# Kernel tuning notes

Hardware: AMD Instinct MI355X
Metric: run time of the kernel (lower is better)

## Reference

```python
import jax, jax.numpy as jnp
import numpy as np

N, E, IN, H, C = 50000, 1600000, 256, 256, 2


def _lin(k, o, i):
    return (jax.random.normal(k, (o, i), jnp.float32) / np.sqrt(i)).astype(jnp.float32)


def setup_inputs() -> dict:
    key = jax.random.key(0)
    ks = jax.random.split(key, 16)
    x = jax.random.normal(ks[0], (N, IN), jnp.float32)
    edge_index = jax.random.randint(ks[1], (2, E), 0, N, dtype=jnp.int32)
    return dict(
        x=x, edge_index=edge_index,
        W1=_lin(ks[2], H, IN), b1=0.01 * jax.random.normal(ks[10], (H,), jnp.float32),
        W2=_lin(ks[3], H, H), b2=0.01 * jax.random.normal(ks[11], (H,), jnp.float32),
        W3=_lin(ks[4], H, H), b3=0.01 * jax.random.normal(ks[12], (H,), jnp.float32),
        W4=_lin(ks[5], C, H), b4=0.01 * jax.random.normal(ks[13], (C,), jnp.float32),
        T10=_lin(ks[6], H, H), T11=_lin(ks[7], H, H), cb1=0.01 * jax.random.normal(ks[14], (H,), jnp.float32),
        T20=_lin(ks[8], H, H), T21=_lin(ks[9], H, H), cb2=0.01 * jax.random.normal(ks[15], (H,), jnp.float32),
    )


def _cheb_norm(edge_index, n):
    # PyG ChebConv, normalization='sym', lambda_max=2.0:
    # L_hat = 2/lambda_max * (I - D^-1/2 A D^-1/2) - I = -D^-1/2 A D^-1/2
    # (the +I and -I self-loop terms cancel), so only off-diagonal norm remains.
    row, col = edge_index[0], edge_index[1]
    deg = jax.ops.segment_sum(jnp.ones((edge_index.shape[1],), jnp.float32), row, num_segments=n)
    dis = jnp.where(deg > 0, jax.lax.rsqrt(jnp.where(deg > 0, deg, 1.0)), 0.0)
    return -dis[row] * dis[col]  # [E]


def _cheb_conv(x, edge_index, norm, W0, W1, b, n):
    # K=2: out = Tx_0 @ W0^T + Tx_1 @ W1^T + b, Tx_0 = x, Tx_1 = L_hat x
    src, dst = edge_index[0], edge_index[1]  # message: x_j from src, aggregate at dst
    tx1 = jax.ops.segment_sum(norm[:, None] * x[src], dst, num_segments=n)
    return x @ W0.T + tx1 @ W1.T + b


def reference(x, edge_index, W1, b1, W2, b2, W3, b3, W4, b4, T10, T11, cb1, T20, T21, cb2):
    n = x.shape[0]
    norm = _cheb_norm(edge_index, n)
    h = jax.nn.relu(x @ W1.T + b1)
    h = jax.nn.relu(h @ W2.T + b2)
    h = _cheb_conv(h, edge_index, norm, T10, T11, cb1, n)
    h = _cheb_conv(h, edge_index, norm, T20, T21, cb2, n)
    h = jax.nn.relu(h @ W3.T + b3)
    return h @ W4.T + b4
```

## Files before the change

kernel.cpp:

```cpp
#include <hip/hip_runtime.h>

#define HDIM 256
#define NHB 256
#define NBINB 50048
#define NBINW (NBINB/4)
#define NBAND 16
#define LDP 40

typedef __attribute__((ext_vector_type(8))) short short8v;
typedef __attribute__((ext_vector_type(4))) short short4v;
typedef __attribute__((ext_vector_type(4))) float floatx4;

static __device__ __forceinline__ unsigned short f2bf(float f) {
    union { float f; unsigned u; } c; c.f = f;
    unsigned u = c.u;
    unsigned r = u + 0x7FFFu + ((u >> 16) & 1u);
    return (unsigned short)(r >> 16);
}
static __device__ __forceinline__ float bf2f(unsigned short h) {
    union { unsigned u; float f; } c; c.u = ((unsigned)h) << 16;
    return c.f;
}


__global__ __launch_bounds__(512) void hist_k(const int* __restrict__ src, const int* __restrict__ dst,
                                              unsigned int* __restrict__ degS, unsigned int* __restrict__ cntS,
                                              int nE) {
    __shared__ unsigned int h8[NBINW];
    const int tid = threadIdx.x;
    const int isDst = blockIdx.x >= NHB;
    const int bb = isDst ? blockIdx.x - NHB : blockIdx.x;
    const int* __restrict__ arr = isDst ? dst : src;
    unsigned int* __restrict__ outS = isDst ? cntS : degS;

    for (int i = tid; i < NBINW; i += 512) h8[i] = 0u;
    __syncthreads();
    const int chunk = (nE + NHB - 1) / NHB;
    const int e0 = bb * chunk;
    const int e1 = min(e0 + chunk, nE);
    for (int e = e0 + tid; e < e1; e += 512) {
        int n = arr[e];
        atomicAdd(&h8[n >> 2], 1u << ((n & 3) << 3));
    }
    __syncthreads();
    unsigned int* __restrict__ row = outS + (size_t)bb * NBINW;
    for (int i = tid; i < NBINW; i += 512) row[i] = h8[i];
}


__global__ __launch_bounds__(256) void reduce_k(const unsigned char* __restrict__ degS,
                                                unsigned char* __restrict__ cntS,
                                                float* __restrict__ dis, int* __restrict__ tmp,
                                                int* __restrict__ bsums, int nN) {
    __shared__ int s[256];
    const int t = threadIdx.x;
    const int n = blockIdx.x * 256 + t;
    int run = 0;
    if (n < nN) {
        int d = 0;
        #pragma unroll 8
        for (int b = 0; b < NHB; ++b) d += degS[(size_t)b * NBINB + n];
        dis[n] = (d > 0) ? (1.0f / sqrtf((float)d)) : 0.0f;
        unsigned r = 0;
        #pragma unroll 4
        for (int b = 0; b < NHB; ++b) {
            size_t o = (size_t)b * NBINB + n;
            unsigned c = cntS[o];
            cntS[o] = (unsigned char)r;
            r += c;
        }
        run = (int)r;
    }
    s[t] = run; __syncthreads();
    #pragma unroll
    for (int off = 1; off < 256; off <<= 1) {
        int x = (t >= off) ? s[t - off] : 0;
        __syncthreads();
        s[t] += x;
        __syncthreads();
    }
    if (n < nN) tmp[n] = s[t];
    if (t == 255) bsums[blockIdx.x] = s[255];
}


__global__ __launch_bounds__(256) void scan3_k(const int* __restrict__ tmp, const int* __restrict__ bsums,
                                               int* __restrict__ offs, int nN, int nE, int nb) {
    __shared__ int s[256];
    const int t = threadIdx.x;
    int v = (t < nb) ? bsums[t] : 0;
    s[t] = v; __syncthreads();
    #pragma unroll
    for (int off = 1; off < 256; off <<= 1) {
        int x = (t >= off) ? s[t - off] : 0;
        __syncthreads();
        s[t] += x;
        __syncthreads();
    }
    const int base = (blockIdx.x > 0) ? s[blockIdx.x - 1] : 0;
    __syncthreads();
    const int i = blockIdx.x * 256 + t;
    if (i < nN) {
        int prev = (t > 0) ? tmp[i - 1] : 0;
        offs[i] = base + prev;
    }
    if (i == nN - 1) offs[nN] = nE;
}


__global__ __launch_bounds__(512) void fill_k(const int* __restrict__ src, const int* __restrict__ dst,
                                              const float* __restrict__ dis, const int* __restrict__ offs,
                                              const unsigned int* __restrict__ cntS,
                                              int2* __restrict__ csr, int nE) {
    __shared__ unsigned int cur8[NBINW];
    const int tid = threadIdx.x;
    const int bb = blockIdx.x;
    const unsigned int* __restrict__ baseRow = cntS + (size_t)bb * NBINW;
    for (int i = tid; i < NBINW; i += 512) cur8[i] = baseRow[i];
    __syncthreads();
    const int chunk = (nE + NHB - 1) / NHB;
    const int e0 = bb * chunk;
    const int e1 = min(e0 + chunk, nE);
    for (int e = e0 + tid; e < e1; e += 512) {
        int s = src[e], d = dst[e];
        unsigned sh = (unsigned)(d & 3) << 3;
        unsigned old = atomicAdd(&cur8[d >> 2], 1u << sh);
        unsigned c = (old >> sh) & 0xFFu;
        int p = offs[d] + (int)c;
        float w = -dis[s] * dis[d];
        csr[p] = make_int2(s, __float_as_int(w));
    }
}


struct WPtrs { const float* w[7]; };
__global__ __launch_bounds__(256) void wsplit_all_k(WPtrs ws, unsigned short* __restrict__ base) {
    int wi = blockIdx.x >> 6;
    int idx = (blockIdx.x & 63) * 256 + threadIdx.x;
    const float* w = ws.w[wi];
    unsigned short* hi = base + (size_t)wi * 131072;
    unsigned short* lo = hi + 65536;
    float4 v = ((const float4*)w)[idx];
    float f[4] = {v.x, v.y, v.z, v.w};
    short4v hv, lv;
    #pragma unroll
    for (int e = 0; e < 4; ++e) {
        unsigned short h = f2bf(f[e]);
        float rem = f[e] - bf2f(h);
        hv[e] = (short)h;
        lv[e] = (short)f2bf(rem);
    }
    *(short4v*)(hi + idx * 4) = hv;
    *(short4v*)(lo + idx * 4) = lv;
}


__global__ __launch_bounds__(512, 4) void mfma_gemm_k(
    const float* __restrict__ AF,
    const unsigned short* __restrict__ Ah0, const unsigned short* __restrict__ Al0,
    const unsigned short* __restrict__ Wh0, const unsigned short* __restrict__ Wl0,
    const unsigned short* __restrict__ Ah1, const unsigned short* __restrict__ Al1,
    const unsigned short* __restrict__ Wh1, const unsigned short* __restrict__ Wl1,
    const float* __restrict__ bias,
    float* __restrict__ outF, unsigned short* __restrict__ outHi, unsigned short* __restrict__ outLo,
    signed char* __restrict__ outI8, float* __restrict__ outSc,
    const float* __restrict__ W4f, const float* __restrict__ b4f, float* __restrict__ outFinal,
    int nRows, int relu, int dual)
{
    __shared__ short Ahs[128 * LDP];
    __shared__ short Als[128 * LDP];
    __shared__ short Bhs[256 * LDP];
    __shared__ short Bls[256 * LDP];

    const int tid  = threadIdx.x;
    const int lane = tid & 63;
    const int wv   = tid >> 6;
    const int wm   = wv >> 2, wn = wv & 3;
    const int lrow = lane & 15, kg = lane >> 4;
    const int row0 = blockIdx.x * 128;

    const int sr = tid >> 2, sc = tid & 3;
    int agr = row0 + sr; if (agr >= nRows) agr = nRows - 1;

    floatx4 acc[4][4];
    #pragma unroll
    for (int i = 0; i < 4; ++i)
        #pragma unroll
        for (int j = 0; j < 4; ++j)
            acc[i][j] = (floatx4)0.0f;

    const int npass = dual ? 2 : 1;
    for (int pass = 0; pass < npass; ++pass) {
        const unsigned short* __restrict__ Ah = pass ? Ah1 : Ah0;
        const unsigned short* __restrict__ Al = pass ? Al1 : Al0;
        const unsigned short* __restrict__ Wh = pass ? Wh1 : Wh0;
        const unsigned short* __restrict__ Wl = pass ? Wl1 : Wl0;
        const bool f32A = (pass == 0) && (AF != nullptr);
        for (int k0 = 0; k0 < HDIM; k0 += 32) {
            __syncthreads();
            if (f32A) {
                const float* pa = AF + (size_t)agr * HDIM + k0 + sc * 8;
                float4 v0 = *(const float4*)pa;
                float4 v1 = *(const float4*)(pa + 4);
                float f[8] = {v0.x, v0.y, v0.z, v0.w, v1.x, v1.y, v1.z, v1.w};
                short8v hv, lv;
                #pragma unroll
                for (int e = 0; e < 8; ++e) {
                    unsigned short h = f2bf(f[e]);
                    float rem = f[e] - bf2f(h);
                    hv[e] = (short)h;
                    lv[e] = (short)f2bf(rem);
                }
                *(short8v*)(Ahs + sr * LDP + sc * 8) = hv;
                *(short8v*)(Als + sr * LDP + sc * 8) = lv;
            } else {
                size_t ga = (size_t)agr * HDIM + k0 + sc * 8;
                *(short8v*)(Ahs + sr * LDP + sc * 8) = *(const short8v*)(Ah + ga);
                *(short8v*)(Als + sr * LDP + sc * 8) = *(const short8v*)(Al + ga);
            }
            #pragma unroll
            for (int q = 0; q < 2; ++q) {
                int idx = tid + q * 512;
                int br = idx >> 2, bc = idx & 3;
                size_t gb = (size_t)br * HDIM + k0 + bc * 8;
                *(short8v*)(Bhs + br * LDP + bc * 8) = *(const short8v*)(Wh + gb);
                *(short8v*)(Bls + br * LDP + bc * 8) = *(const short8v*)(Wl + gb);
            }
            __syncthreads();

            short8v ahf[4], alf[4];
            #pragma unroll
            for (int fm = 0; fm < 4; ++fm) {
                int ra = (wm * 64 + fm * 16 + lrow) * LDP + kg * 8;
                ahf[fm] = *(const short8v*)(Ahs + ra);
                alf[fm] = *(const short8v*)(Als + ra);
            }
            #pragma unroll
            for (int fn = 0; fn < 4; ++fn) {
                int rb = (wn * 64 + fn * 16 + lrow) * LDP + kg * 8;
                short8v bh = *(const short8v*)(Bhs + rb);
                short8v bl = *(const short8v*)(Bls + rb);
                #pragma unroll
                for (int fm = 0; fm < 4; ++fm) {
                    acc[fm][fn] = __builtin_amdgcn_mfma_f32_16x16x32_bf16(ahf[fm], bh, acc[fm][fn], 0, 0, 0);
                    acc[fm][fn] = __builtin_amdgcn_mfma_f32_16x16x32_bf16(ahf[fm], bl, acc[fm][fn], 0, 0, 0);
                    acc[fm][fn] = __builtin_amdgcn_mfma_f32_16x16x32_bf16(alf[fm], bh, acc[fm][fn], 0, 0, 0);
                }
            }
        }
    }

    if (outFinal) {
        float w40[4], w41[4];
        #pragma unroll
        for (int fn = 0; fn < 4; ++fn) {
            int col = wn * 64 + fn * 16 + lrow;
            w40[fn] = W4f[col];
            w41[fn] = W4f[HDIM + col];
        }
        float p0[4][4], p1[4][4];
        #pragma unroll
        for (int fm = 0; fm < 4; ++fm)
            #pragma unroll
            for (int r = 0; r < 4; ++r) { p0[fm][r] = 0.f; p1[fm][r] = 0.f; }
        #pragma unroll
        for (int fn = 0; fn < 4; ++fn) {
            int col = wn * 64 + fn * 16 + lrow;
            float bv = bias[col];
            #pragma unroll
            for (int fm = 0; fm < 4; ++fm)
                #pragma unroll
                for (int r = 0; r < 4; ++r) {
                    float v = fmaxf(acc[fm][fn][r] + bv, 0.0f);
                    p0[fm][r] = fmaf(v, w40[fn], p0[fm][r]);
                    p1[fm][r] = fmaf(v, w41[fn], p1[fm][r]);
                }
        }
        #pragma unroll
        for (int fm = 0; fm < 4; ++fm)
            #pragma unroll
            for (int r = 0; r < 4; ++r) {
                #pragma unroll
                for (int m = 1; m < 16; m <<= 1) {
                    p0[fm][r] += __shfl_xor(p0[fm][r], m, 64);
                    p1[fm][r] += __shfl_xor(p1[fm][r], m, 64);
                }
            }
        __syncthreads();
        float* red = (float*)Ahs;
        if (lrow == 0) {
            #pragma unroll
            for (int fm = 0; fm < 4; ++fm)
                #pragma unroll
                for (int r = 0; r < 4; ++r) {
                    int rl = wm * 64 + fm * 16 + kg * 4 + r;
                    red[(wn * 128 + rl) * 2 + 0] = p0[fm][r];
                    red[(wn * 128 + rl) * 2 + 1] = p1[fm][r];
                }
        }
        __syncthreads();
        if (tid < 256) {
            int rl = tid >> 1, j = tid & 1;
            int grow = row0 + rl;
            if (grow < nRows) {
                float s = b4f[j]
                        + red[(0 * 128 + rl) * 2 + j] + red[(1 * 128 + rl) * 2 + j]
                        + red[(2 * 128 + rl) * 2 + j] + red[(3 * 128 + rl) * 2 + j];
                outFinal[(size_t)grow * 2 + j] = s;
            }
        }
        return;
    }

    float vmax[4][4];
    #pragma unroll
    for (int fm = 0; fm < 4; ++fm)
        #pragma unroll
        for (int r = 0; r < 4; ++r) vmax[fm][r] = 0.0f;
    #pragma unroll
    for (int fn = 0; fn < 4; ++fn) {
        int col = wn * 64 + fn * 16 + lrow;
        float bv = bias[col];
        #pragma unroll
        for (int fm = 0; fm < 4; ++fm) {
            #pragma unroll
            for (int r = 0; r < 4; ++r) {
                float v = acc[fm][fn][r] + bv;
                if (relu) v = fmaxf(v, 0.0f);
                vmax[fm][r] = fmaxf(vmax[fm][r], fabsf(v));
                int grow = row0 + wm * 64 + fm * 16 + kg * 4 + r;
                if (grow < nRows) {
                    size_t o = (size_t)grow * HDIM + col;
                    if (outF) outF[o] = v;
                    if (outHi) {
                        unsigned short h = f2bf(v);
                        outHi[o] = h;
                        outLo[o] = f2bf(v - bf2f(h));
                    }
                }
            }
        }
    }

    if (outI8) {
        #pragma unroll
        for (int fm = 0; fm < 4; ++fm)
            #pragma unroll
            for (int r = 0; r < 4; ++r) {
                #pragma unroll
                for (int m = 1; m < 16; m <<= 1)
                    vmax[fm][r] = fmaxf(vmax[fm][r], __shfl_xor(vmax[fm][r], m, 64));
            }
        __syncthreads();
        float* wmax = (float*)Ahs;
        if (lrow == 0) {
            #pragma unroll
            for (int fm = 0; fm < 4; ++fm)
                #pragma unroll
                for (int r = 0; r < 4; ++r) {
                    int rl = wm * 64 + fm * 16 + kg * 4 + r;
                    wmax[wn * 128 + rl] = vmax[fm][r];
                }
        }
        __syncthreads();
        #pragma unroll
        for (int fm = 0; fm < 4; ++fm) {
            #pragma unroll
            for (int r = 0; r < 4; ++r) {
                int rl = wm * 64 + fm * 16 + kg * 4 + r;
                int grow = row0 + rl;
                float rmax = fmaxf(fmaxf(wmax[rl], wmax[128 + rl]),
                                   fmaxf(wmax[256 + rl], wmax[384 + rl]));
                float inv = (rmax > 0.0f) ? (127.0f / rmax) : 0.0f;
                if (grow < nRows) {
                    #pragma unroll
                    for (int fn = 0; fn < 4; ++fn) {
                        int col = wn * 64 + fn * 16 + lrow;
                        float v = acc[fm][fn][r] + bias[col];
                        if (relu) v = fmaxf(v, 0.0f);
                        outI8[(size_t)grow * HDIM + col] = (signed char)(int)rintf(v * inv);
                    }
                    if (wn == 0 && lrow == 0) outSc[grow] = rmax * (1.0f / 127.0f);
                }
            }
        }
    }
}


#define ACCQ1(m)                                                                 \
    {                                                                            \
        unsigned pv = *(const unsigned*)(hq + (size_t)m.x * HDIM + lane * 4);    \
        float wq = __int_as_float(m.y) * hs[m.x];                                \
        a0 = fmaf(wq, (float)((int)(pv << 24) >> 24), a0);                       \
        a1 = fmaf(wq, (float)((int)(pv << 16) >> 24), a1);                       \
        a2 = fmaf(wq, (float)((int)(pv << 8) >> 24), a2);                        \
        a3 = fmaf(wq, (float)((int)pv >> 24), a3);                               \
    }

#define ACCQ4(m0, m1, m2, m3) { ACCQ1(m0); ACCQ1(m1); ACCQ1(m2); ACCQ1(m3); }

__global__ __launch_bounds__(256) void aggregate_k(
    const signed char* __restrict__ hq, const float* __restrict__ hs,
    const int2* __restrict__ csr, const int* __restrict__ offs,
    unsigned short* __restrict__ outHi, unsigned short* __restrict__ outLo)
{
    __shared__ float red[4][256];
    __shared__ int2 sorted[256];
    __shared__ unsigned bins[NBAND];
    __shared__ unsigned cur[NBAND];

    const int n = blockIdx.x;
    const int tid = threadIdx.x;
    const int w = tid >> 6;
    const int lane = tid & 63;
    const int start = offs[n], end = offs[n + 1];
    const int deg = end - start;

    float a0 = 0.f, a1 = 0.f, a2 = 0.f, a3 = 0.f;

    if (deg <= 256) {
        if (tid < NBAND) { bins[tid] = 0u; }
        __syncthreads();
        int2 my; int myband = 0;
        if (tid < deg) {
            my = csr[start + tid];
            myband = my.x >> 12;
            atomicAdd(&bins[myband], 1u);
        }
        __syncthreads();
        if (tid == 0) {
            unsigned run = 0;
            #pragma unroll
            for (int b = 0; b < NBAND; ++b) { unsigned c = bins[b]; cur[b] = run; run += c; }
        }
        __syncthreads();
        if (tid < deg) {
            unsigned pos = atomicAdd(&cur[myband], 1u);
            sorted[pos] = my;
        }
        __syncthreads();

        int e = w;
        for (; e + 12 < deg; e += 16) {
            int2 m0 = sorted[e], m1 = sorted[e + 4], m2 = sorted[e + 8], m3 = sorted[e + 12];
            ACCQ4(m0, m1, m2, m3);
        }
        for (; e < deg; e += 4) {
            int2 m = sorted[e];
            ACCQ1(m);
        }
    } else {
        int e = start + w;
        for (; e + 12 < end; e += 16) {
            int2 m0 = csr[e], m1 = csr[e + 4], m2 = csr[e + 8], m3 = csr[e + 12];
            ACCQ4(m0, m1, m2, m3);
        }
        for (; e < end; e += 4) {
            int2 m = csr[e];
            ACCQ1(m);
        }
    }

    red[w][lane * 4 + 0] = a0;
    red[w][lane * 4 + 1] = a1;
    red[w][lane * 4 + 2] = a2;
    red[w][lane * 4 + 3] = a3;
    __syncthreads();

    const int t = threadIdx.x;
    float s = red[0][t] + red[1][t] + red[2][t] + red[3][t];
    size_t o = (size_t)n * HDIM + t;
    unsigned short h = f2bf(s);
    outHi[o] = h;
    outLo[o] = f2bf(s - bf2f(h));
}


extern "C" void kernel_launch(void* const* d_in, const int* in_sizes, int n_in,
                              void* d_out, int out_size, void* d_ws, size_t ws_size,
                              hipStream_t stream) {
    const float* x   = (const float*)d_in[0];
    const int*   ei  = (const int*)d_in[1];
    const float* W1  = (const float*)d_in[2];
    const float* b1  = (const float*)d_in[3];
    const float* W2  = (const float*)d_in[4];
    const float* b2  = (const float*)d_in[5];
    const float* W3  = (const float*)d_in[6];
    const float* b3  = (const float*)d_in[7];
    const float* W4  = (const float*)d_in[8];
    const float* b4  = (const float*)d_in[9];
    const float* T10 = (const float*)d_in[10];
    const float* T11 = (const float*)d_in[11];
    const float* cb1 = (const float*)d_in[12];
    const float* T20 = (const float*)d_in[13];
    const float* T21 = (const float*)d_in[14];
    const float* cb2 = (const float*)d_in[15];

    const int nN = in_sizes[0] / HDIM;
    const int nE = in_sizes[1] / 2;
    const int* src = ei;
    const int* dst = ei + nE;

    char* p = (char*)d_ws;
    auto alloc = [&](size_t bytes) { void* r = (void*)p; p += (bytes + 255) & ~(size_t)255; return r; };
    float* dis     = (float*)alloc((size_t)nN * 4);
    int*   tmp     = (int*)alloc((size_t)nN * 4);
    int*   bsums   = (int*)alloc(1024 * 4);
    int*   offs    = (int*)alloc((size_t)(nN + 1) * 4);
    int2*  csr     = (int2*)alloc((size_t)nE * 8);
    unsigned int* degS = (unsigned int*)alloc((size_t)NHB * NBINB);
    unsigned int* cntS = (unsigned int*)alloc((size_t)NHB * NBINB);
    const size_t NH = (size_t)nN * HDIM;
    unsigned short* Xh  = (unsigned short*)alloc(NH * 4);  unsigned short* Xl  = Xh + NH;
    unsigned short* Ahp = (unsigned short*)alloc(NH * 4);  unsigned short* Alp = Ahp + NH;
    unsigned short* Bhp = (unsigned short*)alloc(NH * 4);  unsigned short* Blp = Bhp + NH;
    unsigned short* Dhp = (unsigned short*)alloc(NH * 4);  unsigned short* Dlp = Dhp + NH;
    signed char*    i8b = (signed char*)alloc(NH);
    float*          scb = (float*)alloc((size_t)nN * 4);
    unsigned short* wsp = (unsigned short*)alloc((size_t)7 * 131072 * 2);

    float* out = (float*)d_out;
    const int nbN = (nN + 255) / 256;
    const int gb  = (nN + 127) / 128;

    hist_k<<<2 * NHB, 512, 0, stream>>>(src, dst, degS, cntS, nE);
    reduce_k<<<nbN, 256, 0, stream>>>((const unsigned char*)degS, (unsigned char*)cntS,
                                      dis, tmp, bsums, nN);
    scan3_k<<<nbN, 256, 0, stream>>>(tmp, bsums, offs, nN, nE, nbN);
    fill_k<<<NHB, 512, 0, stream>>>(src, dst, dis, offs, cntS, csr, nE);

    WPtrs wp; wp.w[0]=W1; wp.w[1]=W2; wp.w[2]=T10; wp.w[3]=T11; wp.w[4]=T20; wp.w[5]=T21; wp.w[6]=W3;
    wsplit_all_k<<<7 * 64, 256, 0, stream>>>(wp, wsp);
    unsigned short* wh[7]; unsigned short* wl[7];
    for (int i = 0; i < 7; ++i) { wh[i] = wsp + (size_t)i * 131072; wl[i] = wh[i] + 65536; }

    mfma_gemm_k<<<gb, 512, 0, stream>>>(x, nullptr, nullptr, wh[0], wl[0],
                                        nullptr, nullptr, nullptr, nullptr,
                                        b1, nullptr, Ahp, Alp, nullptr, nullptr,
                                        nullptr, nullptr, nullptr, nN, 1, 0);
    mfma_gemm_k<<<gb, 512, 0, stream>>>(nullptr, Ahp, Alp, wh[1], wl[1],
                                        nullptr, nullptr, nullptr, nullptr,
                                        b2, nullptr, Bhp, Blp, i8b, scb,
                                        nullptr, nullptr, nullptr, nN, 1, 0);

    aggregate_k<<<nN, 256, 0, stream>>>(i8b, scb, csr, offs, Xh, Xl);
    mfma_gemm_k<<<gb, 512, 0, stream>>>(nullptr, Bhp, Blp, wh[2], wl[2],
                                        Xh, Xl, wh[3], wl[3],
                                        cb1, nullptr, Dhp, Dlp, i8b, scb,
                                        nullptr, nullptr, nullptr, nN, 0, 1);

    aggregate_k<<<nN, 256, 0, stream>>>(i8b, scb, csr, offs, Ahp, Alp);
    mfma_gemm_k<<<gb, 512, 0, stream>>>(nullptr, Dhp, Dlp, wh[4], wl[4],
                                        Ahp, Alp, wh[5], wl[5],
                                        cb2, nullptr, Bhp, Blp, nullptr, nullptr,
                                        nullptr, nullptr, nullptr, nN, 0, 1);

    mfma_gemm_k<<<gb, 512, 0, stream>>>(nullptr, Bhp, Blp, wh[6], wl[6],
                                        nullptr, nullptr, nullptr, nullptr,
                                        b3, nullptr, nullptr, nullptr, nullptr, nullptr,
                                        W4, b4, out, nN, 1, 0);
}
```

Baseline: 591.5 us.

## Prefetch next K-step global tiles into registers during MFMA compute

Flattens the pass/k loops of the split-bf16 GEMM into one step loop. The global loads for the next step are issued into registers before the current step's MFMAs run, and stored to LDS at the start of the following iteration. This is meant to hide global memory latency behind compute, at the cost of extra registers that may reduce occupancy.

```diff
diff --git a/kernel.cpp b/kernel.cpp
--- a/kernel.cpp
+++ b/kernel.cpp
@@ -189,63 +189,93 @@
         for (int j = 0; j < 4; ++j)
             acc[i][j] = (floatx4)0.0f;
 
-    const int npass = dual ? 2 : 1;
-    for (int pass = 0; pass < npass; ++pass) {
+    const int nstep = (dual ? 2 : 1) * 8;
+
+    short8v pAh, pAl, pB0h, pB0l, pB1h, pB1l;
+    float4 pF0, pF1;
+
+    auto LOADSTEP = [&](int st) {
+        const int pass = st >> 3;
+        const int k0 = (st & 7) * 32;
         const unsigned short* __restrict__ Ah = pass ? Ah1 : Ah0;
         const unsigned short* __restrict__ Al = pass ? Al1 : Al0;
         const unsigned short* __restrict__ Wh = pass ? Wh1 : Wh0;
         const unsigned short* __restrict__ Wl = pass ? Wl1 : Wl0;
-        const bool f32A = (pass == 0) && (AF != nullptr);
-        for (int k0 = 0; k0 < HDIM; k0 += 32) {
-            __syncthreads();
-            if (f32A) {
-                const float* pa = AF + (size_t)agr * HDIM + k0 + sc * 8;
-                float4 v0 = *(const float4*)pa;
-                float4 v1 = *(const float4*)(pa + 4);
-                float f[8] = {v0.x, v0.y, v0.z, v0.w, v1.x, v1.y, v1.z, v1.w};
-                short8v hv, lv;
-                #pragma unroll
-                for (int e = 0; e < 8; ++e) {
-                    unsigned short h = f2bf(f[e]);
-                    float rem = f[e] - bf2f(h);
-                    hv[e] = (short)h;
-                    lv[e] = (short)f2bf(rem);
-                }
-                *(short8v*)(Ahs + sr * LDP + sc * 8) = hv;
-                *(short8v*)(Als + sr * LDP + sc * 8) = lv;
-            } else {
-                size_t ga = (size_t)agr * HDIM + k0 + sc * 8;
-                *(short8v*)(Ahs + sr * LDP + sc * 8) = *(const short8v*)(Ah + ga);
-                *(short8v*)(Als + sr * LDP + sc * 8) = *(const short8v*)(Al + ga);
-            }
-            #pragma unroll
-            for (int q = 0; q < 2; ++q) {
-                int idx = tid + q * 512;
-                int br = idx >> 2, bc = idx & 3;
-                size_t gb = (size_t)br * HDIM + k0 + bc * 8;
-                *(short8v*)(Bhs + br * LDP + bc * 8) = *(const short8v*)(Wh + gb);
-                *(short8v*)(Bls + br * LDP + bc * 8) = *(const short8v*)(Wl + gb);
-            }
-            __syncthreads();
-
-            short8v ahf[4], alf[4];
+        if ((pass == 0) && (AF != nullptr)) {
+            const float* paf = AF + (size_t)agr * HDIM + k0 + sc * 8;
+            pF0 = *(const float4*)paf;
+            pF1 = *(const float4*)(paf + 4);
+        } else {
+            size_t ga = (size_t)agr * HDIM + k0 + sc * 8;
+            pAh = *(const short8v*)(Ah + ga);
+            pAl = *(const short8v*)(Al + ga);
+        }
+        {
+            int br = tid >> 2, bc = tid & 3;
+            size_t gb = (size_t)br * HDIM + k0 + bc * 8;
+            pB0h = *(const short8v*)(Wh + gb);
+            pB0l = *(const short8v*)(Wl + gb);
+        }
+        {
+            int idx = tid + 512;
+            int br = idx >> 2, bc = idx & 3;
+            size_t gb = (size_t)br * HDIM + k0 + bc * 8;
+            pB1h = *(const short8v*)(Wh + gb);
+            pB1l = *(const short8v*)(Wl + gb);
+        }
+    };
+
+    LOADSTEP(0);
+    for (int st = 0; st < nstep; ++st) {
+        const bool f32A = ((st >> 3) == 0) && (AF != nullptr);
+        __syncthreads();
+        if (f32A) {
+            float f[8] = {pF0.x, pF0.y, pF0.z, pF0.w, pF1.x, pF1.y, pF1.z, pF1.w};
+            short8v hv, lv;
+            #pragma unroll
+            for (int e = 0; e < 8; ++e) {
+                unsigned short h = f2bf(f[e]);
+                float rem = f[e] - bf2f(h);
+                hv[e] = (short)h;
+                lv[e] = (short)f2bf(rem);
+            }
+            *(short8v*)(Ahs + sr * LDP + sc * 8) = hv;
+            *(short8v*)(Als + sr * LDP + sc * 8) = lv;
+        } else {
+            *(short8v*)(Ahs + sr * LDP + sc * 8) = pAh;
+            *(short8v*)(Als + sr * LDP + sc * 8) = pAl;
+        }
+        {
+            int br = tid >> 2, bc = tid & 3;
+            *(short8v*)(Bhs + br * LDP + bc * 8) = pB0h;
+            *(short8v*)(Bls + br * LDP + bc * 8) = pB0l;
+        }
+        {
+            int idx = tid + 512;
+            int br = idx >> 2, bc = idx & 3;
+            *(short8v*)(Bhs + br * LDP + bc * 8) = pB1h;
+            *(short8v*)(Bls + br * LDP + bc * 8) = pB1l;
+        }
+        if (st + 1 < nstep) LOADSTEP(st + 1);
+        __syncthreads();
+
+        short8v ahf[4], alf[4];
+        #pragma unroll
+        for (int fm = 0; fm < 4; ++fm) {
+            int ra = (wm * 64 + fm * 16 + lrow) * LDP + kg * 8;
+            ahf[fm] = *(const short8v*)(Ahs + ra);
+            alf[fm] = *(const short8v*)(Als + ra);
+        }
+        #pragma unroll
+        for (int fn = 0; fn < 4; ++fn) {
+            int rb = (wn * 64 + fn * 16 + lrow) * LDP + kg * 8;
+            short8v bh = *(const short8v*)(Bhs + rb);
+            short8v bl = *(const short8v*)(Bls + rb);
             #pragma unroll
             for (int fm = 0; fm < 4; ++fm) {
-                int ra = (wm * 64 + fm * 16 + lrow) * LDP + kg * 8;
-                ahf[fm] = *(const short8v*)(Ahs + ra);
-                alf[fm] = *(const short8v*)(Als + ra);
-            }
-            #pragma unroll
-            for (int fn = 0; fn < 4; ++fn) {
-                int rb = (wn * 64 + fn * 16 + lrow) * LDP + kg * 8;
-                short8v bh = *(const short8v*)(Bhs + rb);
-                short8v bl = *(const short8v*)(Bls + rb);
-                #pragma unroll
-                for (int fm = 0; fm < 4; ++fm) {
-                    acc[fm][fn] = __builtin_amdgcn_mfma_f32_16x16x32_bf16(ahf[fm], bh, acc[fm][fn], 0, 0, 0);
-                    acc[fm][fn] = __builtin_amdgcn_mfma_f32_16x16x32_bf16(ahf[fm], bl, acc[fm][fn], 0, 0, 0);
-                    acc[fm][fn] = __builtin_amdgcn_mfma_f32_16x16x32_bf16(alf[fm], bh, acc[fm][fn], 0, 0, 0);
-                }
+                acc[fm][fn] = __builtin_amdgcn_mfma_f32_16x16x32_bf16(ahf[fm], bh, acc[fm][fn], 0, 0, 0);
+                acc[fm][fn] = __builtin_amdgcn_mfma_f32_16x16x32_bf16(ahf[fm], bl, acc[fm][fn], 0, 0, 0);
+                acc[fm][fn] = __builtin_amdgcn_mfma_f32_16x16x32_bf16(alf[fm], bh, acc[fm][fn], 0, 0, 0);
             }
         }
     }
```

Result: slower. 955.6 us (+61.6%).
